# Kernel optimization log

Hardware: AMD Instinct MI355X
Metric: run time of the kernel (lower is better)

Reference implementation:

```python
import jax, jax.numpy as jnp
import numpy as np

CUT_SIZE = 224
CUTN = 128
CUT_POW = 1.0
H = W = 1024


def setup_inputs() -> dict:
    key = jax.random.key(0)
    k1, k2, k3, k4 = jax.random.split(key, 4)
    x = jax.random.normal(k1, (1, 3, H, W), dtype=jnp.float32)
    max_size = min(H, W)
    min_size = min(H, W, CUT_SIZE)
    u = jax.random.uniform(k2, (CUTN,))
    # size = int(rand()**cut_pow * (max_size - min_size) + min_size)
    sizes = (u ** CUT_POW * (max_size - min_size) + min_size).astype(jnp.int32)
    # offsets uniform in [0, side - size] inclusive
    oy = jax.random.randint(k3, (CUTN,), 0, H - sizes + 1).astype(jnp.int32)
    ox = jax.random.randint(k4, (CUTN,), 0, W - sizes + 1).astype(jnp.int32)
    return {"input": x, "sizes": sizes, "oy": oy, "ox": ox}


def _cutouts(x, sizes, oy, ox):
    B, C, h, w = x.shape
    cs = CUT_SIZE
    # summed-area table with zero border: I[b,c,r,col] = sum of x[:, :, :r, :col]
    I = jnp.pad(jnp.cumsum(jnp.cumsum(x, axis=2), axis=3),
                ((0, 0), (0, 0), (1, 0), (1, 0)))  # [B,C,h+1,w+1]
    i = jnp.arange(cs, dtype=jnp.int32)
    s = sizes[:, None]                                  # [N,1]
    # adaptive_avg_pool2d bin edges: [floor(i*S/cs), ceil((i+1)*S/cs))
    lo = (i[None, :] * s) // cs                         # [N,cs]
    hi = -((-(i[None, :] + 1) * s) // cs)               # ceil via neg-floor
    r0 = oy[:, None] + lo
    r1 = oy[:, None] + hi
    c0 = ox[:, None] + lo
    c1 = ox[:, None] + hi
    # rectangle sums for all cutouts/output pixels: [B,C,N,cs,cs]
    S = (I[:, :, r1[:, :, None], c1[:, None, :]]
         - I[:, :, r0[:, :, None], c1[:, None, :]]
         - I[:, :, r1[:, :, None], c0[:, None, :]]
         + I[:, :, r0[:, :, None], c0[:, None, :]])
    area = ((r1 - r0)[:, :, None] * (c1 - c0)[:, None, :]).astype(x.dtype)  # [N,cs,cs]
    out = S / area[None, None]                          # [B,C,N,cs,cs]
    # torch.cat(cutouts) over dim 0 -> [N*B, C, cs, cs]
    return jnp.transpose(out, (2, 0, 1, 3, 4)).reshape(CUTN * B, C, cs, cs)


def reference(input, sizes, oy, ox):
    return _cutouts(input, sizes, oy, ox)
```

## Files before the change

kernel.cpp:

```cpp
#include <hip/hip_runtime.h>

#define CS   224
#define HH   1024
#define WW   1024
#define HW   (HH * WW)
#define RT   16
#define NTIL (HH / RT)
#define NCOLG 2
#define ROWS 4

__global__ __launch_bounds__(256) void row_cumsum(
    const float* __restrict__ x, float* __restrict__ I)
{
    int row = blockIdx.x;
    const float4* src = (const float4*)(x + (size_t)row * WW);
    float4*       dst = (float4*)(I + (size_t)row * WW);

    int t    = threadIdx.x;
    int lane = t & 63;
    int w    = t >> 6;

    float4 v = src[t];
    float s0 = v.x, s1 = s0 + v.y, s2 = s1 + v.z, s3 = s2 + v.w;
    float tsum = s3, sc = tsum;
    #pragma unroll
    for (int d = 1; d < 64; d <<= 1) {
        float o = __shfl_up(sc, d, 64);
        if (lane >= d) sc += o;
    }

    __shared__ float wsum[4];
    if (lane == 63) wsum[w] = sc;
    __syncthreads();
    float woff = 0.0f;
    #pragma unroll
    for (int k = 0; k < 4; ++k) woff += (k < w) ? wsum[k] : 0.0f;

    float ex = woff + sc - tsum;
    dst[t] = make_float4(ex + s0, ex + s1, ex + s2, ex + s3);
}

__global__ __launch_bounds__(256) void col_sum(
    const float* __restrict__ I, float* __restrict__ Sf)
{
    int b    = blockIdx.x;
    int tile = b % NTIL;
    int cg   = (b / NTIL) % NCOLG;
    int ch   = b / (NTIL * NCOLG);
    int c2   = cg * 256 + threadIdx.x;

    const float2* base = (const float2*)(I + (size_t)ch * HW
                                           + (size_t)(tile * RT) * WW) + c2;
    float2 acc = make_float2(0.0f, 0.0f);
    #pragma unroll
    for (int r = 0; r < RT; ++r) {
        float2 v = base[(size_t)r * (WW / 2)];
        acc.x += v.x; acc.y += v.y;
    }
    ((float2*)Sf)[(size_t)(ch * NTIL + tile) * (WW / 2) + c2] = acc;
}

__global__ __launch_bounds__(256) void scan_S(float* __restrict__ Sf)
{
    int gw   = (blockIdx.x * 256 + threadIdx.x) >> 6;
    int lane = threadIdx.x & 63;
    int c    = gw % WW;
    int ch   = gw / WW;

    size_t idx = ((size_t)(ch * NTIL + lane)) * WW + c;
    float v = Sf[idx];
    #pragma unroll
    for (int d = 1; d < 64; d <<= 1) {
        float o = __shfl_up(v, d, 64);
        if (lane >= d) v += o;
    }
    Sf[idx] = v;
}

__global__ __launch_bounds__(256) void col_apply(
    float* __restrict__ I, const float* __restrict__ Sf)
{
    int b    = blockIdx.x;
    int tile = b % NTIL;
    int cg   = (b / NTIL) % NCOLG;
    int ch   = b / (NTIL * NCOLG);
    int c2   = cg * 256 + threadIdx.x;

    float2 acc = make_float2(0.0f, 0.0f);
    if (tile > 0)
        acc = ((const float2*)Sf)[(size_t)(ch * NTIL + tile - 1) * (WW / 2) + c2];

    float2* base = (float2*)(I + (size_t)ch * HW + (size_t)(tile * RT) * WW) + c2;
    #pragma unroll
    for (int r = 0; r < RT; ++r) {
        float2 v = base[(size_t)r * (WW / 2)];
        acc.x += v.x; acc.y += v.y;
        base[(size_t)r * (WW / 2)] = acc;
    }
}

__global__ __launch_bounds__(256) void cutouts_gather(
    const float* __restrict__ I,
    const int*   __restrict__ sizesv,
    const int*   __restrict__ oyv,
    const int*   __restrict__ oxv,
    float*       __restrict__ out)
{
    int b   = blockIdx.x;
    int rg  = b % (CS / ROWS);
    int rem = b / (CS / ROWS);
    int n   = rem % 128;
    int ch  = rem / 128;

    int j = threadIdx.x;
    if (j >= CS) return;

    int s   = sizesv[n];
    int oy_ = oyv[n];
    int ox_ = oxv[n];

    int lo_j = (j * s) / CS;
    int hi_j = ((j + 1) * s + (CS - 1)) / CS;
    int c0   = ox_ + lo_j;
    int bcol = ox_ + hi_j - 1;
    bool am  = (c0 > 0);
    int acol = am ? (c0 - 1) : 0;
    float rcpC = __builtin_amdgcn_rcpf((float)(hi_j - lo_j));

    const float* Ic = I + (size_t)ch * HW;

    const float* rowHi[ROWS];
    const float* rowLo[ROWS];
    bool  rmv[ROWS];
    float rcpA[ROWS];
    #pragma unroll
    for (int rr = 0; rr < ROWS; ++rr) {
        int i    = rg * ROWS + rr;
        int lo_i = (i * s) / CS;
        int nR   = ((i + 1) * s + (CS - 1)) / CS - lo_i;
        int r0   = oy_ + lo_i;
        int r1m  = r0 + nR - 1;
        bool rm  = (r0 > 0);
        int r0m  = rm ? (r0 - 1) : 0;
        rowHi[rr] = Ic + (size_t)r1m * WW;
        rowLo[rr] = Ic + (size_t)r0m * WW;
        rmv[rr]   = rm;
        rcpA[rr]  = rcpC * __builtin_amdgcn_rcpf((float)nR);
    }

    float vhb[ROWS], vha[ROWS], vlb[ROWS], vla[ROWS];
    #pragma unroll
    for (int rr = 0; rr < ROWS; ++rr) {
        vhb[rr] = rowHi[rr][bcol];
        vha[rr] = rowHi[rr][acol];
        vlb[rr] = rowLo[rr][bcol];
        vla[rr] = rowLo[rr][acol];
    }

    #pragma unroll
    for (int rr = 0; rr < ROWS; ++rr) {
        int i = rg * ROWS + rr;
        float sum = vhb[rr]
                  - (am ? vha[rr] : 0.0f)
                  - (rmv[rr] ? vlb[rr] : 0.0f)
                  + ((am && rmv[rr]) ? vla[rr] : 0.0f);
        out[((size_t)((n * 3 + ch) * CS) + i) * CS + j] = sum * rcpA[rr];
    }
}

extern "C" void kernel_launch(void* const* d_in, const int* in_sizes, int n_in,
                              void* d_out, int out_size, void* d_ws, size_t ws_size,
                              hipStream_t stream) {
    const float* x     = (const float*)d_in[0];
    const int*   sizes = (const int*)d_in[1];
    const int*   oy    = (const int*)d_in[2];
    const int*   ox    = (const int*)d_in[3];
    float*       out   = (float*)d_out;
    float*       I     = (float*)d_ws;

    float* S = out + (out_size - 3 * NTIL * WW);

    row_cumsum<<<3 * HH, 256, 0, stream>>>(x, I);
    col_sum<<<3 * NCOLG * NTIL, 256, 0, stream>>>(I, S);
    scan_S<<<(3 * WW) / 4, 256, 0, stream>>>(S);
    col_apply<<<3 * NCOLG * NTIL, 256, 0, stream>>>(I, S);

    int blocks = 3 * 128 * (CS / ROWS);
    cutouts_gather<<<blocks, 256, 0, stream>>>(I, sizes, oy, ox, out);
}
```

Baseline: 69.87 us.

## Vectorize cutout gather with per-thread column pairs and window loads

Each gather thread now produces two adjacent output columns and loads a contiguous window of the integral image with vector loads, choosing the needed corner values through a template specialised on size/CS. Each block covers 8 rows split across two thread halves, and the output is written as float2. The integral image is offset by 16 bytes in the workspace so that reading the column before the window (acol = -1) stays in bounds. The aim is fewer scattered scalar gather instructions and more coalesced stores, in exchange for more select logic, a larger register footprint, and unaligned vector loads.

```diff
diff --git a/kernel.cpp b/kernel.cpp
--- a/kernel.cpp
+++ b/kernel.cpp
@@ -7,7 +7,11 @@
 #define RT   16
 #define NTIL (HH / RT)
 #define NCOLG 2
-#define ROWS 4
+#define RWS  8
+
+typedef float f4u __attribute__((ext_vector_type(4), aligned(4)));
+typedef float f2u __attribute__((ext_vector_type(2), aligned(4)));
+typedef float f2s __attribute__((ext_vector_type(2), aligned(8)));
 
 __global__ __launch_bounds__(256) void row_cumsum(
     const float* __restrict__ x, float* __restrict__ I)
@@ -96,6 +100,101 @@
         float2 v = base[(size_t)r * (WW / 2)];
         acc.x += v.x; acc.y += v.y;
         base[(size_t)r * (WW / 2)] = acc;
+    }
+}
+
+template<int K0>
+__device__ __forceinline__ void ldwin(const float* __restrict__ p, float v[12])
+{
+    f4u q0 = *(const f4u*)p;
+    v[0] = q0.x; v[1] = q0.y; v[2] = q0.z; v[3] = q0.w;
+    if constexpr (K0 == 1) {
+        f2u e = *(const f2u*)(p + 4);
+        v[4] = e.x; v[5] = e.y;
+    } else if constexpr (K0 == 2) {
+        f4u q1 = *(const f4u*)(p + 4);
+        v[4] = q1.x; v[5] = q1.y; v[6] = q1.z; v[7] = q1.w;
+    } else if constexpr (K0 == 3) {
+        f4u q1 = *(const f4u*)(p + 4);
+        v[4] = q1.x; v[5] = q1.y; v[6] = q1.z; v[7] = q1.w;
+        f2u e = *(const f2u*)(p + 8);
+        v[8] = e.x; v[9] = e.y;
+    } else {
+        f4u q1 = *(const f4u*)(p + 4);
+        v[4] = q1.x; v[5] = q1.y; v[6] = q1.z; v[7] = q1.w;
+        f4u q2 = *(const f4u*)(p + 8);
+        v[8] = q2.x; v[9] = q2.y; v[10] = q2.z; v[11] = q2.w;
+    }
+}
+
+template<int K0>
+__device__ __forceinline__ float selB0(const float v[12], int nC0) {
+    float r = v[K0];
+    r = (nC0 == K0 + 1) ? v[K0 + 1] : r;
+    r = (nC0 == K0 + 2) ? v[K0 + 2] : r;
+    return r;
+}
+template<int K0>
+__device__ __forceinline__ float selA1(const float v[12], int d) {
+    return (d == K0) ? v[K0] : v[K0 + 1];
+}
+template<int K0>
+__device__ __forceinline__ float selB1(const float v[12], int db) {
+    float r = v[2 * K0];
+    r = (db == 2 * K0 + 1) ? v[2 * K0 + 1] : r;
+    r = (db == 2 * K0 + 2) ? v[2 * K0 + 2] : r;
+    r = (db == 2 * K0 + 3) ? v[2 * K0 + 3] : r;
+    return r;
+}
+
+template<int K0>
+__device__ __forceinline__ void gather_impl(
+    const float* __restrict__ Ic, int s, int oy_, int ox_,
+    int rg, int p, int ro, float* __restrict__ outrowbase)
+{
+    int j0 = 2 * p;
+    int j1 = j0 + 1;
+    int lo0 = (j0 * s) / CS;
+    int hi0 = ((j0 + 1) * s + CS - 1) / CS;
+    int lo1 = (j1 * s) / CS;
+    int hi1 = ((j1 + 1) * s + CS - 1) / CS;
+    int nC0 = hi0 - lo0;
+    int nC1 = hi1 - lo1;
+    int d   = lo1 - lo0;
+    int db  = d + nC1;
+    int acol = ox_ + lo0 - 1;
+    bool am0 = (ox_ + lo0) > 0;
+    float rC0 = __builtin_amdgcn_rcpf((float)nC0);
+    float rC1 = __builtin_amdgcn_rcpf((float)nC1);
+
+    #pragma unroll
+    for (int rr = 0; rr < RWS / 2; ++rr) {
+        int i    = rg * RWS + ro + 2 * rr;
+        int lo_i = (i * s) / CS;
+        int nR   = ((i + 1) * s + CS - 1) / CS - lo_i;
+        int r0   = oy_ + lo_i;
+        int r1m  = r0 + nR - 1;
+        bool rm  = (r0 > 0);
+        int r0m  = rm ? (r0 - 1) : 0;
+
+        float vh[12], vl[12];
+        ldwin<K0>(Ic + (size_t)r1m * WW + acol, vh);
+        ldwin<K0>(Ic + (size_t)r0m * WW + acol, vl);
+
+        float ah0 = vh[0],            al0 = vl[0];
+        float bh0 = selB0<K0>(vh, nC0), bl0 = selB0<K0>(vl, nC0);
+        float ah1 = selA1<K0>(vh, d),   al1 = selA1<K0>(vl, d);
+        float bh1 = selB1<K0>(vh, db),  bl1 = selB1<K0>(vl, db);
+
+        float s0 = (bh0 - (am0 ? ah0 : 0.0f))
+                 - (rm ? (bl0 - (am0 ? al0 : 0.0f)) : 0.0f);
+        float s1 = (bh1 - ah1) - (rm ? (bl1 - al1) : 0.0f);
+
+        float rR = __builtin_amdgcn_rcpf((float)nR);
+        f2s st;
+        st.x = s0 * (rC0 * rR);
+        st.y = s1 * (rC1 * rR);
+        *(f2s*)(outrowbase + (size_t)i * CS + j0) = st;
     }
 }
 
@@ -107,65 +206,28 @@
     float*       __restrict__ out)
 {
     int b   = blockIdx.x;
-    int rg  = b % (CS / ROWS);
-    int rem = b / (CS / ROWS);
+    int rg  = b % (CS / RWS);
+    int rem = b / (CS / RWS);
     int n   = rem % 128;
     int ch  = rem / 128;
 
-    int j = threadIdx.x;
-    if (j >= CS) return;
+    int tid = threadIdx.x;
+    int p   = tid & 127;
+    int ro  = tid >> 7;
+    if (p >= 112) return;
 
     int s   = sizesv[n];
     int oy_ = oyv[n];
     int ox_ = oxv[n];
 
-    int lo_j = (j * s) / CS;
-    int hi_j = ((j + 1) * s + (CS - 1)) / CS;
-    int c0   = ox_ + lo_j;
-    int bcol = ox_ + hi_j - 1;
-    bool am  = (c0 > 0);
-    int acol = am ? (c0 - 1) : 0;
-    float rcpC = __builtin_amdgcn_rcpf((float)(hi_j - lo_j));
-
     const float* Ic = I + (size_t)ch * HW;
-
-    const float* rowHi[ROWS];
-    const float* rowLo[ROWS];
-    bool  rmv[ROWS];
-    float rcpA[ROWS];
-    #pragma unroll
-    for (int rr = 0; rr < ROWS; ++rr) {
-        int i    = rg * ROWS + rr;
-        int lo_i = (i * s) / CS;
-        int nR   = ((i + 1) * s + (CS - 1)) / CS - lo_i;
-        int r0   = oy_ + lo_i;
-        int r1m  = r0 + nR - 1;
-        bool rm  = (r0 > 0);
-        int r0m  = rm ? (r0 - 1) : 0;
-        rowHi[rr] = Ic + (size_t)r1m * WW;
-        rowLo[rr] = Ic + (size_t)r0m * WW;
-        rmv[rr]   = rm;
-        rcpA[rr]  = rcpC * __builtin_amdgcn_rcpf((float)nR);
-    }
-
-    float vhb[ROWS], vha[ROWS], vlb[ROWS], vla[ROWS];
-    #pragma unroll
-    for (int rr = 0; rr < ROWS; ++rr) {
-        vhb[rr] = rowHi[rr][bcol];
-        vha[rr] = rowHi[rr][acol];
-        vlb[rr] = rowLo[rr][bcol];
-        vla[rr] = rowLo[rr][acol];
-    }
-
-    #pragma unroll
-    for (int rr = 0; rr < ROWS; ++rr) {
-        int i = rg * ROWS + rr;
-        float sum = vhb[rr]
-                  - (am ? vha[rr] : 0.0f)
-                  - (rmv[rr] ? vlb[rr] : 0.0f)
-                  + ((am && rmv[rr]) ? vla[rr] : 0.0f);
-        out[((size_t)((n * 3 + ch) * CS) + i) * CS + j] = sum * rcpA[rr];
-    }
+    float* outrowbase = out + (size_t)((n * 3 + ch) * CS) * CS;
+
+    int k0 = s / CS;
+    if      (k0 == 1) gather_impl<1>(Ic, s, oy_, ox_, rg, p, ro, outrowbase);
+    else if (k0 == 2) gather_impl<2>(Ic, s, oy_, ox_, rg, p, ro, outrowbase);
+    else if (k0 == 3) gather_impl<3>(Ic, s, oy_, ox_, rg, p, ro, outrowbase);
+    else              gather_impl<4>(Ic, s, oy_, ox_, rg, p, ro, outrowbase);
 }
 
 extern "C" void kernel_launch(void* const* d_in, const int* in_sizes, int n_in,
@@ -176,7 +238,8 @@
     const int*   oy    = (const int*)d_in[2];
     const int*   ox    = (const int*)d_in[3];
     float*       out   = (float*)d_out;
-    float*       I     = (float*)d_ws;
+
+    float* I = (float*)((char*)d_ws + 16);
 
     float* S = out + (out_size - 3 * NTIL * WW);
 
@@ -185,6 +248,6 @@
     scan_S<<<(3 * WW) / 4, 256, 0, stream>>>(S);
     col_apply<<<3 * NCOLG * NTIL, 256, 0, stream>>>(I, S);
 
-    int blocks = 3 * 128 * (CS / ROWS);
+    int blocks = 3 * 128 * (CS / RWS);
     cutouts_gather<<<blocks, 256, 0, stream>>>(I, sizes, oy, ox, out);
 }
```

After: 123.7 us. 1.77x slower.

## Replace 2D summed-area table with column prefix sums and direct horizontal bin sums

Applied to the files above, without the earlier changes.

Drops the row cumsum pass and builds only a vertical prefix sum V over the input. The gather kernel then forms each bin sum by subtracting two rows of V and summing the bin's 1-6 columns directly, using vector loads specialised on s/CS. This removes one full read and write pass over the image, and it replaces four scattered SAT lookups with two short contiguous reads. In exchange, the gather reads more elements per output and relies on unaligned vector loads that may run past the bin or the image edge.

```diff
diff --git a/kernel.cpp b/kernel.cpp
--- a/kernel.cpp
+++ b/kernel.cpp
@@ -9,39 +9,11 @@
 #define NCOLG 2
 #define ROWS 4
 
-__global__ __launch_bounds__(256) void row_cumsum(
-    const float* __restrict__ x, float* __restrict__ I)
-{
-    int row = blockIdx.x;
-    const float4* src = (const float4*)(x + (size_t)row * WW);
-    float4*       dst = (float4*)(I + (size_t)row * WW);
-
-    int t    = threadIdx.x;
-    int lane = t & 63;
-    int w    = t >> 6;
-
-    float4 v = src[t];
-    float s0 = v.x, s1 = s0 + v.y, s2 = s1 + v.z, s3 = s2 + v.w;
-    float tsum = s3, sc = tsum;
-    #pragma unroll
-    for (int d = 1; d < 64; d <<= 1) {
-        float o = __shfl_up(sc, d, 64);
-        if (lane >= d) sc += o;
-    }
-
-    __shared__ float wsum[4];
-    if (lane == 63) wsum[w] = sc;
-    __syncthreads();
-    float woff = 0.0f;
-    #pragma unroll
-    for (int k = 0; k < 4; ++k) woff += (k < w) ? wsum[k] : 0.0f;
-
-    float ex = woff + sc - tsum;
-    dst[t] = make_float4(ex + s0, ex + s1, ex + s2, ex + s3);
-}
+typedef float f4u __attribute__((ext_vector_type(4), aligned(4)));
+typedef float f2u __attribute__((ext_vector_type(2), aligned(4)));
 
 __global__ __launch_bounds__(256) void col_sum(
-    const float* __restrict__ I, float* __restrict__ Sf)
+    const float* __restrict__ x, float* __restrict__ Sf)
 {
     int b    = blockIdx.x;
     int tile = b % NTIL;
@@ -49,7 +21,7 @@
     int ch   = b / (NTIL * NCOLG);
     int c2   = cg * 256 + threadIdx.x;
 
-    const float2* base = (const float2*)(I + (size_t)ch * HW
+    const float2* base = (const float2*)(x + (size_t)ch * HW
                                            + (size_t)(tile * RT) * WW) + c2;
     float2 acc = make_float2(0.0f, 0.0f);
     #pragma unroll
@@ -78,7 +50,8 @@
 }
 
 __global__ __launch_bounds__(256) void col_apply(
-    float* __restrict__ I, const float* __restrict__ Sf)
+    const float* __restrict__ x, const float* __restrict__ Sf,
+    float* __restrict__ V)
 {
     int b    = blockIdx.x;
     int tile = b % NTIL;
@@ -90,17 +63,70 @@
     if (tile > 0)
         acc = ((const float2*)Sf)[(size_t)(ch * NTIL + tile - 1) * (WW / 2) + c2];
 
-    float2* base = (float2*)(I + (size_t)ch * HW + (size_t)(tile * RT) * WW) + c2;
+    const float2* src = (const float2*)(x + (size_t)ch * HW
+                                          + (size_t)(tile * RT) * WW) + c2;
+    float2*       dst = (float2*)(V + (size_t)ch * HW
+                                    + (size_t)(tile * RT) * WW) + c2;
     #pragma unroll
     for (int r = 0; r < RT; ++r) {
-        float2 v = base[(size_t)r * (WW / 2)];
+        float2 v = src[(size_t)r * (WW / 2)];
         acc.x += v.x; acc.y += v.y;
-        base[(size_t)r * (WW / 2)] = acc;
+        dst[(size_t)r * (WW / 2)] = acc;
+    }
+}
+
+template<int K0>
+__device__ __forceinline__ void gather_impl(
+    const float* __restrict__ Vc, int s, int oy_, int ox_,
+    int rg, int j, float* __restrict__ ob)
+{
+    int lo_j = (j * s) / CS;
+    int hi_j = ((j + 1) * s + CS - 1) / CS;
+    int nC   = hi_j - lo_j;
+    int c0   = ox_ + lo_j;
+    float rcpC = __builtin_amdgcn_rcpf((float)nC);
+
+    #pragma unroll
+    for (int rr = 0; rr < ROWS; ++rr) {
+        int i    = rg * ROWS + rr;
+        int lo_i = (i * s) / CS;
+        int nR   = ((i + 1) * s + CS - 1) / CS - lo_i;
+        int r0   = oy_ + lo_i;
+        int r1m  = r0 + nR - 1;
+        bool rm  = (r0 > 0);
+        int r0m  = rm ? (r0 - 1) : 0;
+
+        const float* Rhi = Vc + (size_t)r1m * WW + c0;
+        const float* Rlo = Vc + (size_t)r0m * WW + c0;
+
+        f4u qh = *(const f4u*)Rhi;
+        f4u ql = *(const f4u*)Rlo;
+        float sh, sl;
+        if constexpr (K0 == 1) {
+            sh = qh.x + (nC >= 2 ? qh.y : 0.0f) + (nC >= 3 ? qh.z : 0.0f);
+            sl = ql.x + (nC >= 2 ? ql.y : 0.0f) + (nC >= 3 ? ql.z : 0.0f);
+        } else if constexpr (K0 == 2) {
+            sh = qh.x + qh.y + (nC >= 3 ? qh.z : 0.0f) + (nC >= 4 ? qh.w : 0.0f);
+            sl = ql.x + ql.y + (nC >= 3 ? ql.z : 0.0f) + (nC >= 4 ? ql.w : 0.0f);
+        } else if constexpr (K0 == 3) {
+            float eh = Rhi[4], el = Rlo[4];
+            sh = qh.x + qh.y + qh.z + (nC >= 4 ? qh.w : 0.0f) + (nC >= 5 ? eh : 0.0f);
+            sl = ql.x + ql.y + ql.z + (nC >= 4 ? ql.w : 0.0f) + (nC >= 5 ? el : 0.0f);
+        } else {
+            f2u eh = *(const f2u*)(Rhi + 4);
+            f2u el = *(const f2u*)(Rlo + 4);
+            sh = qh.x + qh.y + qh.z + qh.w + (nC >= 5 ? eh.x : 0.0f) + (nC >= 6 ? eh.y : 0.0f);
+            sl = ql.x + ql.y + ql.z + ql.w + (nC >= 5 ? el.x : 0.0f) + (nC >= 6 ? el.y : 0.0f);
+        }
+
+        float sum  = sh - (rm ? sl : 0.0f);
+        float rcpR = __builtin_amdgcn_rcpf((float)nR);
+        ob[(size_t)i * CS + j] = sum * (rcpC * rcpR);
     }
 }
 
 __global__ __launch_bounds__(256) void cutouts_gather(
-    const float* __restrict__ I,
+    const float* __restrict__ V,
     const int*   __restrict__ sizesv,
     const int*   __restrict__ oyv,
     const int*   __restrict__ oxv,
@@ -119,53 +145,14 @@
     int oy_ = oyv[n];
     int ox_ = oxv[n];
 
-    int lo_j = (j * s) / CS;
-    int hi_j = ((j + 1) * s + (CS - 1)) / CS;
-    int c0   = ox_ + lo_j;
-    int bcol = ox_ + hi_j - 1;
-    bool am  = (c0 > 0);
-    int acol = am ? (c0 - 1) : 0;
-    float rcpC = __builtin_amdgcn_rcpf((float)(hi_j - lo_j));
+    const float* Vc = V + (size_t)ch * HW;
+    float* ob = out + (size_t)((n * 3 + ch) * CS) * CS;
 
-    const float* Ic = I + (size_t)ch * HW;
-
-    const float* rowHi[ROWS];
-    const float* rowLo[ROWS];
-    bool  rmv[ROWS];
-    float rcpA[ROWS];
-    #pragma unroll
-    for (int rr = 0; rr < ROWS; ++rr) {
-        int i    = rg * ROWS + rr;
-        int lo_i = (i * s) / CS;
-        int nR   = ((i + 1) * s + (CS - 1)) / CS - lo_i;
-        int r0   = oy_ + lo_i;
-        int r1m  = r0 + nR - 1;
-        bool rm  = (r0 > 0);
-        int r0m  = rm ? (r0 - 1) : 0;
-        rowHi[rr] = Ic + (size_t)r1m * WW;
-        rowLo[rr] = Ic + (size_t)r0m * WW;
-        rmv[rr]   = rm;
-        rcpA[rr]  = rcpC * __builtin_amdgcn_rcpf((float)nR);
-    }
-
-    float vhb[ROWS], vha[ROWS], vlb[ROWS], vla[ROWS];
-    #pragma unroll
-    for (int rr = 0; rr < ROWS; ++rr) {
-        vhb[rr] = rowHi[rr][bcol];
-        vha[rr] = rowHi[rr][acol];
-        vlb[rr] = rowLo[rr][bcol];
-        vla[rr] = rowLo[rr][acol];
-    }
-
-    #pragma unroll
-    for (int rr = 0; rr < ROWS; ++rr) {
-        int i = rg * ROWS + rr;
-        float sum = vhb[rr]
-                  - (am ? vha[rr] : 0.0f)
-                  - (rmv[rr] ? vlb[rr] : 0.0f)
-                  + ((am && rmv[rr]) ? vla[rr] : 0.0f);
-        out[((size_t)((n * 3 + ch) * CS) + i) * CS + j] = sum * rcpA[rr];
-    }
+    int k0 = s / CS;
+    if      (k0 == 1) gather_impl<1>(Vc, s, oy_, ox_, rg, j, ob);
+    else if (k0 == 2) gather_impl<2>(Vc, s, oy_, ox_, rg, j, ob);
+    else if (k0 == 3) gather_impl<3>(Vc, s, oy_, ox_, rg, j, ob);
+    else              gather_impl<4>(Vc, s, oy_, ox_, rg, j, ob);
 }
 
 extern "C" void kernel_launch(void* const* d_in, const int* in_sizes, int n_in,
@@ -176,15 +163,14 @@
     const int*   oy    = (const int*)d_in[2];
     const int*   ox    = (const int*)d_in[3];
     float*       out   = (float*)d_out;
-    float*       I     = (float*)d_ws;
+    float*       V     = (float*)d_ws;
 
     float* S = out + (out_size - 3 * NTIL * WW);
 
-    row_cumsum<<<3 * HH, 256, 0, stream>>>(x, I);
-    col_sum<<<3 * NCOLG * NTIL, 256, 0, stream>>>(I, S);
+    col_sum<<<3 * NCOLG * NTIL, 256, 0, stream>>>(x, S);
     scan_S<<<(3 * WW) / 4, 256, 0, stream>>>(S);
-    col_apply<<<3 * NCOLG * NTIL, 256, 0, stream>>>(I, S);
+    col_apply<<<3 * NCOLG * NTIL, 256, 0, stream>>>(x, S, V);
 
     int blocks = 3 * 128 * (CS / ROWS);
-    cutouts_gather<<<blocks, 256, 0, stream>>>(I, sizes, oy, ox, out);
+    cutouts_gather<<<blocks, 256, 0, stream>>>(V, sizes, oy, ox, out);
 }
```

New measurement: 56.49 us. -19.1%, faster.
